# Optimization experiments

Hardware: AMD Instinct MI355X
Metric: run time of the kernel (lower is better)

## Reference

```python
import jax, jax.numpy as jnp
import numpy as np

D_MODEL = 1024
N_HEADS = 16
D_HEAD = D_MODEL // N_HEADS


def setup_inputs() -> dict:
    key = jax.random.key(0)
    k1, k2, k3, k4, k5 = jax.random.split(key, 5)
    B, S = 2, 2048
    scale_in = 1.0 / np.sqrt(D_MODEL)
    return {
        "x": jax.random.normal(k1, (B, S, D_MODEL), dtype=jnp.float32),
        "qkv_w": jax.random.normal(k2, (3 * D_MODEL, D_MODEL), dtype=jnp.float32) * scale_in,
        "qkv_b": jax.random.normal(k3, (3 * D_MODEL,), dtype=jnp.float32) * 0.02,
        "out_w": jax.random.normal(k4, (D_MODEL, D_MODEL), dtype=jnp.float32) * scale_in,
        "out_b": jax.random.normal(k5, (D_MODEL,), dtype=jnp.float32) * 0.02,
    }


def reference(x, qkv_w, qkv_b, out_w, out_b) -> jnp.ndarray:
    B, S, D = x.shape
    # qkv projection: torch Linear stores weight as (out, in)
    qkv = x @ qkv_w.T + qkv_b                      # [B,S,3D]
    qkv = qkv.reshape(B, S, 3, N_HEADS, D_HEAD)
    qkv = jnp.transpose(qkv, (2, 0, 3, 1, 4))      # [3,B,H,S,d]
    q, k, v = qkv[0], qkv[1], qkv[2]
    scale = 1.0 / np.sqrt(D_HEAD).astype(np.float32)
    scores = jnp.einsum("bhsd,bhtd->bhst", q, k) * scale  # [B,H,S,S]
    attn = jax.nn.softmax(scores, axis=-1)
    out = jnp.einsum("bhst,bhtd->bhsd", attn, v)   # [B,H,S,d]
    out = jnp.transpose(out, (0, 2, 1, 3)).reshape(B, S, D)
    return out @ out_w.T + out_b
```

## Files before the change

### kernel.cpp

```cpp
#include <hip/hip_runtime.h>

typedef __bf16 bf16;
typedef __bf16 bf16x4 __attribute__((ext_vector_type(4)));
typedef __bf16 bf16x8 __attribute__((ext_vector_type(8)));
typedef float  f32x4  __attribute__((ext_vector_type(4)));

__device__ __forceinline__ void gld16(const void* g, void* l) {
  __builtin_amdgcn_global_load_lds(
      (const __attribute__((address_space(1))) void*)g,
      (__attribute__((address_space(3))) void*)l, 16, 0, 0);
}

__global__ void f2bf_all(const float* __restrict__ x, bf16* __restrict__ xo,
                         const float* __restrict__ w1, bf16* __restrict__ w1o,
                         const float* __restrict__ w2, bf16* __restrict__ w2o) {
  int i = blockIdx.x * blockDim.x + threadIdx.x;
  const float* in; bf16* out; int idx;
  if (i < 1048576)      { in = x;  out = xo;  idx = i; }
  else if (i < 1835008) { in = w1; out = w1o; idx = i - 1048576; }
  else                  { in = w2; out = w2o; idx = i - 1835008; }
  float4 v = reinterpret_cast<const float4*>(in)[idx];
  bf16x4 o = { (bf16)v.x, (bf16)v.y, (bf16)v.z, (bf16)v.w };
  reinterpret_cast<bf16x4*>(out)[idx] = o;
}

template<int MODE, int BN>
__global__ __launch_bounds__(256)
void gemm_bt(const bf16* __restrict__ A, const bf16* __restrict__ B,
             const float* __restrict__ bias, void* __restrict__ Cout,
             int K, int N) {
  __shared__ bf16 As[128 * 64];
  __shared__ bf16 Bs[BN * 64];
  const int tid  = threadIdx.x;
  const int wave = tid >> 6, lane = tid & 63;
  const int quad = lane >> 4, l16 = lane & 15;
  const int bm = blockIdx.x * 128, bn = blockIdx.y * BN;
  constexpr int NI  = (BN == 128) ? 4 : 2;
  constexpr int BCH = BN / 32;
  const int wr = (BN == 128) ? (wave >> 1) * 64 : wave * 32;
  const int wc = (BN == 128) ? (wave & 1) * 64 : 0;
  const int arow = lane >> 3;
  const int acol = (lane & 7) * 8;

  f32x4 acc[NI][4] = {};

  const bf16* Ab = A + (size_t)bm * K;
  const bf16* Bb = B + (size_t)bn * K;

  for (int k0 = 0; k0 < K; k0 += 64) {
#pragma unroll
    for (int i = 0; i < 4; ++i) {
      int c = wave * 4 + i;
      gld16(Ab + (size_t)(c * 8 + arow) * K + k0 + acol, As + c * 512);
    }
#pragma unroll
    for (int i = 0; i < BCH; ++i) {
      int c = wave * BCH + i;
      gld16(Bb + (size_t)(c * 8 + arow) * K + k0 + acol, Bs + c * 512);
    }
    __syncthreads();
#pragma unroll
    for (int kk = 0; kk < 64; kk += 32) {
      bf16x8 af[NI], bfr[4];
#pragma unroll
      for (int i = 0; i < NI; ++i)
        af[i]  = *(const bf16x8*)(As + (wr + i * 16 + l16) * 64 + kk + quad * 8);
#pragma unroll
      for (int j = 0; j < 4; ++j)
        bfr[j] = *(const bf16x8*)(Bs + (wc + j * 16 + l16) * 64 + kk + quad * 8);
#pragma unroll
      for (int i = 0; i < NI; ++i)
#pragma unroll
        for (int j = 0; j < 4; ++j)
          acc[i][j] = __builtin_amdgcn_mfma_f32_16x16x32_bf16(af[i], bfr[j], acc[i][j], 0, 0, 0);
    }
    __syncthreads();
  }

  if constexpr (MODE == 0) {
    bf16* Q = (bf16*)Cout;
#pragma unroll
    for (int j = 0; j < 4; ++j) {
      int col = bn + wc + j * 16 + l16;
      float bv  = bias[col];
      int sec = col >> 10, rem = col & 1023;
      int h = rem >> 6, d = rem & 63;
      if (sec < 2) {
        float scl = (sec == 0) ? 0.125f * 1.44269504f : 1.0f;
#pragma unroll
        for (int i = 0; i < NI; ++i) {
#pragma unroll
          for (int r = 0; r < 4; ++r) {
            int row = bm + wr + i * 16 + quad * 4 + r;
            int b = row >> 11, si = row & 2047;
            float v = (acc[i][j][r] + bv) * scl;
            Q[(((size_t)sec * 32 + b * 16 + h) * 2048 + si) * 64 + d] = (bf16)v;
          }
        }
      } else {
#pragma unroll
        for (int i = 0; i < NI; ++i) {
          int row0 = bm + wr + i * 16 + quad * 4;
          int b = row0 >> 11, si = row0 & 2047;
          bf16x4 pk = { (bf16)(acc[i][j][0] + bv), (bf16)(acc[i][j][1] + bv),
                        (bf16)(acc[i][j][2] + bv), (bf16)(acc[i][j][3] + bv) };
          *(bf16x4*)(Q + (size_t)2 * 4194304 +
                     ((size_t)(b * 16 + h) * 64 + d) * 2048 + si) = pk;
        }
      }
    }
  } else {
    float* C = (float*)Cout;
#pragma unroll
    for (int j = 0; j < 4; ++j) {
      int col = bn + wc + j * 16 + l16;
      float bv = bias[col];
#pragma unroll
      for (int i = 0; i < NI; ++i)
#pragma unroll
        for (int r = 0; r < 4; ++r) {
          int row = bm + wr + i * 16 + quad * 4 + r;
          C[(size_t)row * N + col] = acc[i][j][r] + bv;
        }
    }
  }
}

__global__ __launch_bounds__(256, 2)
void attn_kernel(const bf16* __restrict__ QKV, const bf16* __restrict__ Vt,
                 float* __restrict__ Opart, float* __restrict__ lpart) {
  __shared__ bf16 Ks[128 * 72];
  __shared__ bf16 Ps[4][32 * 72];

  const int bh = blockIdx.x;
  const int q0 = blockIdx.y * 128;
  const int half = blockIdx.z;
  const int kt0 = half * 8;
  const bf16* Qg = QKV + ((size_t)bh * 2048 + q0) * 64;
  const bf16* Kg = QKV + (size_t)32 * 2048 * 64 + (size_t)bh * 2048 * 64;
  const bf16* Vg = Vt + (size_t)bh * 64 * 2048;
  float* Oh = Opart + (size_t)half * 4194304 + (size_t)bh * 2048 * 64;
  float* lh = lpart + (size_t)half * 65536 + (size_t)bh * 2048;

  const int tid  = threadIdx.x;
  const int wave = tid >> 6, lane = tid & 63;
  const int quad = lane >> 4, l16 = lane & 15;
  const int srow = tid >> 3;
  const int scol = (tid & 7) * 8;
  bf16* Pw = &Ps[wave][0];

  bf16x8 aq[2][2];
#pragma unroll
  for (int i = 0; i < 2; ++i)
#pragma unroll
    for (int kh = 0; kh < 2; ++kh)
      aq[i][kh] = *(const bf16x8*)(Qg + (size_t)(wave * 32 + i * 16 + l16) * 64 +
                                   kh * 32 + quad * 8);

  {
    bf16x8 kreg[4];
#pragma unroll
    for (int ch = 0; ch < 4; ++ch)
      kreg[ch] = *(const bf16x8*)(Kg + (size_t)(kt0 * 128 + ch * 32 + srow) * 64 + scol);
#pragma unroll
    for (int ch = 0; ch < 4; ++ch)
      *(bf16x8*)(&Ks[(ch * 32 + srow) * 72 + scol]) = kreg[ch];
  }
  __syncthreads();

  float rs[2] = {0.f, 0.f};
  f32x4 o[2][4] = {};

  for (int kt = 0; kt < 8; ++kt) {
    const int g = kt0 + kt;

    bf16x8 kreg[4];
    if (kt < 7) {
#pragma unroll
      for (int ch = 0; ch < 4; ++ch)
        kreg[ch] = *(const bf16x8*)(Kg + (size_t)((g + 1) * 128 + ch * 32 + srow) * 64 + scol);
    }
    bf16x8 bv[4][4];
#pragma unroll
    for (int kk = 0; kk < 4; ++kk)
#pragma unroll
      for (int oj = 0; oj < 4; ++oj)
        bv[kk][oj] = *(const bf16x8*)(Vg + (size_t)(oj * 16 + l16) * 2048 +
                                      g * 128 + kk * 32 + quad * 8);

    f32x4 s[2][8] = {};
#pragma unroll
    for (int kh = 0; kh < 2; ++kh) {
#pragma unroll
      for (int ni = 0; ni < 8; ++ni) {
        bf16x8 bk = *(const bf16x8*)(&Ks[(ni * 16 + l16) * 72 + kh * 32 + quad * 8]);
        s[0][ni] = __builtin_amdgcn_mfma_f32_16x16x32_bf16(bk, aq[0][kh], s[0][ni], 0, 0, 0);
        s[1][ni] = __builtin_amdgcn_mfma_f32_16x16x32_bf16(bk, aq[1][kh], s[1][ni], 0, 0, 0);
      }
    }

    __syncthreads();

    if (kt < 7) {
#pragma unroll
      for (int ch = 0; ch < 4; ++ch)
        *(bf16x8*)(&Ks[(ch * 32 + srow) * 72 + scol]) = kreg[ch];
    }

#pragma unroll
    for (int c = 0; c < 2; ++c) {
#pragma unroll
      for (int i = 0; i < 2; ++i)
#pragma unroll
        for (int nc = 0; nc < 4; ++nc) {
          int ni = c * 4 + nc;
          float p0 = __builtin_amdgcn_exp2f(s[i][ni][0]);
          float p1 = __builtin_amdgcn_exp2f(s[i][ni][1]);
          float p2 = __builtin_amdgcn_exp2f(s[i][ni][2]);
          float p3 = __builtin_amdgcn_exp2f(s[i][ni][3]);
          rs[i] += (p0 + p1) + (p2 + p3);
          bf16x4 pk = { (bf16)p0, (bf16)p1, (bf16)p2, (bf16)p3 };
          *(bf16x4*)(Pw + (i * 16 + l16) * 72 + nc * 16 + quad * 4) = pk;
        }
#pragma unroll
      for (int kc = 0; kc < 2; ++kc) {
        int kk = c * 2 + kc;
#pragma unroll
        for (int i = 0; i < 2; ++i) {
          bf16x8 ap = *(const bf16x8*)(Pw + (i * 16 + l16) * 72 + kc * 32 + quad * 8);
#pragma unroll
          for (int oj = 0; oj < 4; ++oj)
            o[i][oj] = __builtin_amdgcn_mfma_f32_16x16x32_bf16(ap, bv[kk][oj], o[i][oj], 0, 0, 0);
        }
      }
    }

    __syncthreads();
  }

#pragma unroll
  for (int i = 0; i < 2; ++i) {
    rs[i] += __shfl_xor(rs[i], 16);
    rs[i] += __shfl_xor(rs[i], 32);
  }

#pragma unroll
  for (int i = 0; i < 2; ++i) {
    if (quad == 0)
      lh[q0 + wave * 32 + i * 16 + l16] = rs[i];
#pragma unroll
    for (int r = 0; r < 4; ++r) {
      int row = q0 + wave * 32 + i * 16 + quad * 4 + r;
#pragma unroll
      for (int oj = 0; oj < 4; ++oj)
        Oh[(size_t)row * 64 + oj * 16 + l16] = o[i][oj][r];
    }
  }
}

__global__ void attn_combine(const float* __restrict__ O0, const float* __restrict__ O1,
                             const float* __restrict__ l0, const float* __restrict__ l1,
                             bf16* __restrict__ At) {
  int i = blockIdx.x * blockDim.x + threadIdx.x;
  int rid = i >> 4, d4 = i & 15;
  float inv = 1.0f / (l0[rid] + l1[rid]);
  f32x4 a = reinterpret_cast<const f32x4*>(O0)[i];
  f32x4 b = reinterpret_cast<const f32x4*>(O1)[i];
  int bh = rid >> 11, s = rid & 2047;
  int bb = bh >> 4, h = bh & 15;
  bf16x4 ov = { (bf16)((a[0] + b[0]) * inv), (bf16)((a[1] + b[1]) * inv),
                (bf16)((a[2] + b[2]) * inv), (bf16)((a[3] + b[3]) * inv) };
  *reinterpret_cast<bf16x4*>(At + ((size_t)(bb * 2048 + s)) * 1024 + h * 64 + d4 * 4) = ov;
}

extern "C" void kernel_launch(void* const* d_in, const int* in_sizes, int n_in,
                              void* d_out, int out_size, void* d_ws, size_t ws_size,
                              hipStream_t stream) {
  const float* x      = (const float*)d_in[0];
  const float* qkv_w  = (const float*)d_in[1];
  const float* qkv_b  = (const float*)d_in[2];
  const float* out_w  = (const float*)d_in[3];
  const float* out_b  = (const float*)d_in[4];
  float* out = (float*)d_out;

  char* ws = (char*)d_ws;
  bf16* Xb    = (bf16*)(ws);
  bf16* Wqkv  = (bf16*)(ws + 8388608);
  bf16* Wout  = (bf16*)(ws + 14680064);
  bf16* QKV   = (bf16*)(ws + 16777216);
  bf16* At    = (bf16*)(ws + 41943040);
  float* Opart = (float*)(ws + 50331648);
  float* lpart = (float*)(ws + 83886080);
  bf16* VtP   = QKV + (size_t)2 * 32 * 2048 * 64;

  f2bf_all<<<8192, 256, 0, stream>>>(x, Xb, qkv_w, Wqkv, out_w, Wout);

  gemm_bt<0, 128><<<dim3(32, 24), 256, 0, stream>>>(Xb, Wqkv, qkv_b, (void*)QKV, 1024, 3072);

  attn_kernel<<<dim3(32, 16, 2), 256, 0, stream>>>(QKV, VtP, Opart, lpart);

  attn_combine<<<4096, 256, 0, stream>>>(Opart, Opart + 4194304,
                                         lpart, lpart + 65536, At);

  gemm_bt<1, 64><<<dim3(32, 16), 256, 0, stream>>>(At, Wout, out_b, (void*)out, 1024, 1024);
}
```

Before: 233.4 us.

## Stream K via global_load_lds with XOR-swizzled LDS and split score computation

K tiles are now loaded straight from global into LDS with global_load_lds into an unpadded, XOR-swizzled layout, replacing register staging with a padded layout. The score computation and V register loads are split into two halves per K tile, so only half the score and V registers are live at once. Launch bounds are raised to 3 blocks per SM. The aim is to lower register and LDS pressure for more occupancy while keeping LDS bank conflicts low. In exchange, the next-tile K load now sits behind the second half's barrier, which may expose more load latency.

```diff
diff --git a/kernel.cpp b/kernel.cpp
--- a/kernel.cpp
+++ b/kernel.cpp
@@ -126,10 +126,10 @@
   }
 }
 
-__global__ __launch_bounds__(256, 2)
+__global__ __launch_bounds__(256, 3)
 void attn_kernel(const bf16* __restrict__ QKV, const bf16* __restrict__ Vt,
                  float* __restrict__ Opart, float* __restrict__ lpart) {
-  __shared__ bf16 Ks[128 * 72];
+  __shared__ bf16 Ks[128 * 64];
   __shared__ bf16 Ps[4][32 * 72];
 
   const int bh = blockIdx.x;
@@ -146,7 +146,8 @@
   const int wave = tid >> 6, lane = tid & 63;
   const int quad = lane >> 4, l16 = lane & 15;
   const int srow = tid >> 3;
-  const int scol = (tid & 7) * 8;
+  const int swcol = ((tid & 7) * 8) ^ ((srow & 7) << 3);
+  const int xrd = (l16 & 7) << 3;
   bf16* Pw = &Ps[wave][0];
 
   bf16x8 aq[2][2];
@@ -157,15 +158,10 @@
       aq[i][kh] = *(const bf16x8*)(Qg + (size_t)(wave * 32 + i * 16 + l16) * 64 +
                                    kh * 32 + quad * 8);
 
-  {
-    bf16x8 kreg[4];
-#pragma unroll
-    for (int ch = 0; ch < 4; ++ch)
-      kreg[ch] = *(const bf16x8*)(Kg + (size_t)(kt0 * 128 + ch * 32 + srow) * 64 + scol);
-#pragma unroll
-    for (int ch = 0; ch < 4; ++ch)
-      *(bf16x8*)(&Ks[(ch * 32 + srow) * 72 + scol]) = kreg[ch];
-  }
+#pragma unroll
+  for (int ch = 0; ch < 4; ++ch)
+    gld16(Kg + (size_t)(kt0 * 128 + ch * 32 + srow) * 64 + swcol,
+          Ks + ch * 2048 + wave * 512);
   __syncthreads();
 
   float rs[2] = {0.f, 0.f};
@@ -174,63 +170,59 @@
   for (int kt = 0; kt < 8; ++kt) {
     const int g = kt0 + kt;
 
-    bf16x8 kreg[4];
-    if (kt < 7) {
-#pragma unroll
-      for (int ch = 0; ch < 4; ++ch)
-        kreg[ch] = *(const bf16x8*)(Kg + (size_t)((g + 1) * 128 + ch * 32 + srow) * 64 + scol);
-    }
-    bf16x8 bv[4][4];
-#pragma unroll
-    for (int kk = 0; kk < 4; ++kk)
-#pragma unroll
-      for (int oj = 0; oj < 4; ++oj)
-        bv[kk][oj] = *(const bf16x8*)(Vg + (size_t)(oj * 16 + l16) * 2048 +
-                                      g * 128 + kk * 32 + quad * 8);
-
-    f32x4 s[2][8] = {};
-#pragma unroll
-    for (int kh = 0; kh < 2; ++kh) {
-#pragma unroll
-      for (int ni = 0; ni < 8; ++ni) {
-        bf16x8 bk = *(const bf16x8*)(&Ks[(ni * 16 + l16) * 72 + kh * 32 + quad * 8]);
-        s[0][ni] = __builtin_amdgcn_mfma_f32_16x16x32_bf16(bk, aq[0][kh], s[0][ni], 0, 0, 0);
-        s[1][ni] = __builtin_amdgcn_mfma_f32_16x16x32_bf16(bk, aq[1][kh], s[1][ni], 0, 0, 0);
-      }
-    }
-
-    __syncthreads();
-
-    if (kt < 7) {
-#pragma unroll
-      for (int ch = 0; ch < 4; ++ch)
-        *(bf16x8*)(&Ks[(ch * 32 + srow) * 72 + scol]) = kreg[ch];
-    }
-
 #pragma unroll
     for (int c = 0; c < 2; ++c) {
+      bf16x8 bv[2][4];
+#pragma unroll
+      for (int kc = 0; kc < 2; ++kc)
+#pragma unroll
+        for (int oj = 0; oj < 4; ++oj)
+          bv[kc][oj] = *(const bf16x8*)(Vg + (size_t)(oj * 16 + l16) * 2048 +
+                                        g * 128 + (c * 2 + kc) * 32 + quad * 8);
+
+      f32x4 s[2][4] = {};
+#pragma unroll
+      for (int kh = 0; kh < 2; ++kh) {
+#pragma unroll
+        for (int nc = 0; nc < 4; ++nc) {
+          int row = (c * 4 + nc) * 16 + l16;
+          bf16x8 bk = *(const bf16x8*)(&Ks[row * 64 + ((kh * 32 + quad * 8) ^ xrd)]);
+          s[0][nc] = __builtin_amdgcn_mfma_f32_16x16x32_bf16(bk, aq[0][kh], s[0][nc], 0, 0, 0);
+          s[1][nc] = __builtin_amdgcn_mfma_f32_16x16x32_bf16(bk, aq[1][kh], s[1][nc], 0, 0, 0);
+        }
+      }
+
+      if (c == 1) {
+        __syncthreads();
+        if (kt < 7) {
+#pragma unroll
+          for (int ch = 0; ch < 4; ++ch)
+            gld16(Kg + (size_t)((g + 1) * 128 + ch * 32 + srow) * 64 + swcol,
+                  Ks + ch * 2048 + wave * 512);
+        }
+      }
+
 #pragma unroll
       for (int i = 0; i < 2; ++i)
 #pragma unroll
         for (int nc = 0; nc < 4; ++nc) {
-          int ni = c * 4 + nc;
-          float p0 = __builtin_amdgcn_exp2f(s[i][ni][0]);
-          float p1 = __builtin_amdgcn_exp2f(s[i][ni][1]);
-          float p2 = __builtin_amdgcn_exp2f(s[i][ni][2]);
-          float p3 = __builtin_amdgcn_exp2f(s[i][ni][3]);
+          float p0 = __builtin_amdgcn_exp2f(s[i][nc][0]);
+          float p1 = __builtin_amdgcn_exp2f(s[i][nc][1]);
+          float p2 = __builtin_amdgcn_exp2f(s[i][nc][2]);
+          float p3 = __builtin_amdgcn_exp2f(s[i][nc][3]);
           rs[i] += (p0 + p1) + (p2 + p3);
           bf16x4 pk = { (bf16)p0, (bf16)p1, (bf16)p2, (bf16)p3 };
           *(bf16x4*)(Pw + (i * 16 + l16) * 72 + nc * 16 + quad * 4) = pk;
         }
+
 #pragma unroll
       for (int kc = 0; kc < 2; ++kc) {
-        int kk = c * 2 + kc;
 #pragma unroll
         for (int i = 0; i < 2; ++i) {
           bf16x8 ap = *(const bf16x8*)(Pw + (i * 16 + l16) * 72 + kc * 32 + quad * 8);
 #pragma unroll
           for (int oj = 0; oj < 4; ++oj)
-            o[i][oj] = __builtin_amdgcn_mfma_f32_16x16x32_bf16(ap, bv[kk][oj], o[i][oj], 0, 0, 0);
+            o[i][oj] = __builtin_amdgcn_mfma_f32_16x16x32_bf16(ap, bv[kc][oj], o[i][oj], 0, 0, 0);
         }
       }
     }
```

After: 234.2 us. About the same (+0.3%).
